# Performance work log

Measured on AMD Instinct MI355X. Metric: run time of the kernel, lower is better.

## Reference

```python
import jax, jax.numpy as jnp
import numpy as np

B, T, F, H = 256, 128, 1024, 512  # batch, input_size (time window), feature_dim, hidden_size


def setup_inputs() -> dict:
    key = jax.random.key(0)
    ks = jax.random.split(key, 7)
    in1 = T + 2 * H
    return {
        "h": jax.random.normal(ks[0], (B, H), dtype=jnp.float32),
        "s": jax.random.normal(ks[1], (B, H), dtype=jnp.float32),
        "x": jax.random.normal(ks[2], (B, T, F), dtype=jnp.float32),
        "W1": jax.random.normal(ks[3], (T, in1), dtype=jnp.float32) / np.sqrt(in1),
        "b1": jnp.zeros((T,), dtype=jnp.float32),
        "W2": jax.random.normal(ks[4], (1, T), dtype=jnp.float32) / np.sqrt(T),
        "b2": jnp.zeros((1,), dtype=jnp.float32),
    }


def reference(h, s, x, W1, b1, W2, b2):
    feature_dim = x.shape[-1]
    xp = jnp.transpose(x, (2, 0, 1))                     # [F, B, T]
    hb = jnp.broadcast_to(h[None], (feature_dim,) + h.shape)  # [F, B, H]
    sb = jnp.broadcast_to(s[None], (feature_dim,) + s.shape)  # [F, B, H]
    cat = jnp.concatenate([xp, hb, sb], axis=-1)         # [F, B, T+2H]
    u = jnp.einsum('fbk,tk->fbt', cat, W1) + b1          # [F, B, T]
    e = jnp.einsum('fbt,ot->fbo', jnp.tanh(u), W2) + b2  # [F, B, 1]
    alpha = jax.nn.softmax(e, axis=0)[..., 0]            # softmax over feature dim -> [F, B]
    return alpha.T                                       # [B, F]
```

## Files before the change

### kernel.cpp

```cpp
#include <hip/hip_runtime.h>
#include <hip/hip_bf16.h>


#define B_N 256
#define T_N 128
#define F_N 1024
#define H_N 512
#define IN1 1152

typedef __bf16 bf16x8 __attribute__((ext_vector_type(8)));
typedef float f32x16 __attribute__((ext_vector_type(16)));
typedef float f32x4_t __attribute__((ext_vector_type(4)));
typedef unsigned int u32x4 __attribute__((ext_vector_type(4)));

__device__ __forceinline__ float wave_reduce_sum(float v) {
#pragma unroll
  for (int off = 32; off >= 1; off >>= 1) v += __shfl_xor(v, off, 64);
  return v;
}
__device__ __forceinline__ float wave_reduce_max(float v) {
#pragma unroll
  for (int off = 32; off >= 1; off >>= 1) v = fmaxf(v, __shfl_xor(v, off, 64));
  return v;
}
__device__ __forceinline__ float tanh_fast(float u) {
  u = fminf(fmaxf(u, -15.f), 15.f);
  float e2 = __expf(2.f * u);
  return (e2 - 1.f) / (e2 + 1.f);
}
__device__ __forceinline__ unsigned bfbits(float f) {
  return (unsigned)__builtin_bit_cast(unsigned short, (__bf16)f);
}
__device__ __forceinline__ float dot4(float4 a, float4 b) {
  return a.x * b.x + a.y * b.y + a.z * b.z + a.w * b.w;
}

__global__ __launch_bounds__(256) void kA_c(const float* __restrict__ h,
                                            const float* __restrict__ s,
                                            const float* __restrict__ W1,
                                            const float* __restrict__ b1,
                                            float* __restrict__ c) {
  int tid = threadIdx.x, lane = tid & 63, wave = tid >> 6;
  int t = blockIdx.x >> 2, bq = blockIdx.x & 3;
  const float4* wrow = reinterpret_cast<const float4*>(W1 + (size_t)t * IN1 + T_N);
  float4 w0 = wrow[lane], w1v = wrow[64 + lane], w2v = wrow[128 + lane], w3v = wrow[192 + lane];
  float b1t = b1[t];
  int b0 = bq * 64;
#pragma unroll 2
  for (int bi = 0; bi < 16; ++bi) {
    int b = b0 + wave + bi * 4;
    const float4* hr = reinterpret_cast<const float4*>(h + (size_t)b * H_N);
    const float4* sr = reinterpret_cast<const float4*>(s + (size_t)b * H_N);
    float acc = dot4(w0, hr[lane]) + dot4(w1v, hr[64 + lane]) +
                dot4(w2v, sr[lane]) + dot4(w3v, sr[64 + lane]);
    acc = wave_reduce_sum(acc);
    if (lane == 0) c[(size_t)b * T_N + t] = acc + b1t;
  }
}

__global__ __launch_bounds__(256) void kA_frag(const float* __restrict__ W1,
                                               unsigned short* __restrict__ w1frag) {
  int i = blockIdx.x * 256 + threadIdx.x;
  int p0 = i * 2;
  int j = p0 & 7;
  int lane = (p0 >> 3) & 63;
  int kk = (p0 >> 9) & 7;
  int tt = (p0 >> 12) & 3;
  int t = tt * 32 + (lane & 31);
  int k = kk * 16 + 8 * (lane >> 5) + j;
  const float2 w = *reinterpret_cast<const float2*>(W1 + t * IN1 + k);
  *reinterpret_cast<unsigned*>(w1frag + p0) = bfbits(w.x) | (bfbits(w.y) << 16);
}

__global__ __launch_bounds__(256, 4) void kB_e(const float* __restrict__ x,
                                               const unsigned short* __restrict__ w1frag,
                                               const float* __restrict__ c,
                                               const float* __restrict__ W2,
                                               const float* __restrict__ b2,
                                               float* __restrict__ e) {
  __shared__ __align__(16) unsigned char xlds[32768];
  __shared__ __align__(16) float clds[T_N];
  __shared__ __align__(16) float w2lds[T_N];
  __shared__ __align__(16) float epart[4][T_N];
  int tid = threadIdx.x;
  int b = blockIdx.x >> 3;
  int fc = blockIdx.x & 7;
  const int fbase = fc * 128;

  if (tid < T_N) clds[tid] = c[(size_t)b * T_N + tid];
  else w2lds[tid - T_N] = W2[tid - T_N];

  {
    const float* xb = x + (size_t)b * T_N * F_N + fbase;
#pragma unroll
    for (int i = 0; i < 4; ++i) {
      int u = tid + 256 * i;
      int kq = u >> 5, fq = u & 31;
      const float* base = xb + (size_t)(kq * 4) * F_N + fq * 4;
      float4 r0 = *reinterpret_cast<const float4*>(base);
      float4 r1 = *reinterpret_cast<const float4*>(base + F_N);
      float4 r2 = *reinterpret_cast<const float4*>(base + 2 * F_N);
      float4 r3 = *reinterpret_cast<const float4*>(base + 3 * F_N);
      u32x4 pa, pb;
      pa[0] = bfbits(r0.x) | (bfbits(r1.x) << 16);
      pa[1] = bfbits(r2.x) | (bfbits(r3.x) << 16);
      pa[2] = bfbits(r0.y) | (bfbits(r1.y) << 16);
      pa[3] = bfbits(r2.y) | (bfbits(r3.y) << 16);
      pb[0] = bfbits(r0.z) | (bfbits(r1.z) << 16);
      pb[1] = bfbits(r2.z) | (bfbits(r3.z) << 16);
      pb[2] = bfbits(r0.w) | (bfbits(r1.w) << 16);
      pb[3] = bfbits(r2.w) | (bfbits(r3.w) << 16);
      unsigned char* dst = xlds + kq * 1024 + fq * 32;
      *reinterpret_cast<u32x4*>(dst) = pa;
      *reinterpret_cast<u32x4*>(dst + 16) = pb;
    }
  }
  __syncthreads();

  const int lane = tid & 63, wave = tid >> 6;
  const int g = lane >> 5, l31 = lane & 31;
  const bf16x8* af = reinterpret_cast<const bf16x8*>(w1frag);

  f32x16 acc0 = {}, acc1 = {}, acc2 = {}, acc3 = {};
#pragma unroll 4
  for (int kk = 0; kk < 8; ++kk) {
    bf16x8 afr = af[wave * 512 + kk * 64 + lane];
    const unsigned char* bbase = xlds + (kk * 4 + 2 * g) * 1024 + l31 * 8;
#define BFRAG(C)                                                                    \
  ({                                                                                \
    uint2 lo = *reinterpret_cast<const uint2*>(bbase + (C) * 256);                  \
    uint2 hi = *reinterpret_cast<const uint2*>(bbase + (C) * 256 + 1024);           \
    u32x4 q = {lo.x, lo.y, hi.x, hi.y};                                             \
    __builtin_bit_cast(bf16x8, q);                                                  \
  })
    acc0 = __builtin_amdgcn_mfma_f32_32x32x16_bf16(afr, BFRAG(0), acc0, 0, 0, 0);
    acc1 = __builtin_amdgcn_mfma_f32_32x32x16_bf16(afr, BFRAG(1), acc1, 0, 0, 0);
    acc2 = __builtin_amdgcn_mfma_f32_32x32x16_bf16(afr, BFRAG(2), acc2, 0, 0, 0);
    acc3 = __builtin_amdgcn_mfma_f32_32x32x16_bf16(afr, BFRAG(3), acc3, 0, 0, 0);
#undef BFRAG
  }

  const int tbase = wave * 32 + 4 * g;
  float es0 = 0.f, es1 = 0.f, es2 = 0.f, es3 = 0.f;
#pragma unroll
  for (int q = 0; q < 4; ++q) {
    f32x4_t cq = *reinterpret_cast<const f32x4_t*>(&clds[tbase + 8 * q]);
    f32x4_t wq = *reinterpret_cast<const f32x4_t*>(&w2lds[tbase + 8 * q]);
#pragma unroll
    for (int r = 0; r < 4; ++r) {
      int reg = q * 4 + r;
      es0 += wq[r] * tanh_fast(acc0[reg] + cq[r]);
      es1 += wq[r] * tanh_fast(acc1[reg] + cq[r]);
      es2 += wq[r] * tanh_fast(acc2[reg] + cq[r]);
      es3 += wq[r] * tanh_fast(acc3[reg] + cq[r]);
    }
  }
  es0 += __shfl_xor(es0, 32, 64);
  es1 += __shfl_xor(es1, 32, 64);
  es2 += __shfl_xor(es2, 32, 64);
  es3 += __shfl_xor(es3, 32, 64);
  if (g == 0) {
    epart[wave][l31] = es0;
    epart[wave][32 + l31] = es1;
    epart[wave][64 + l31] = es2;
    epart[wave][96 + l31] = es3;
  }
  __syncthreads();
  if (tid < T_N) {
    e[(size_t)b * F_N + fbase + tid] =
        epart[0][tid] + epart[1][tid] + epart[2][tid] + epart[3][tid] + b2[0];
  }
}

__global__ __launch_bounds__(256) void kC_softmax(float* __restrict__ out) {
  int b = blockIdx.x, tid = threadIdx.x;
  int lane = tid & 63, wid = tid >> 6;
  float* row = out + (size_t)b * F_N;
  float v[4];
#pragma unroll
  for (int q = 0; q < 4; ++q) v[q] = row[tid + 256 * q];
  float m = fmaxf(fmaxf(v[0], v[1]), fmaxf(v[2], v[3]));
  m = wave_reduce_max(m);
  __shared__ float rm[4], rs[4];
  if (lane == 0) rm[wid] = m;
  __syncthreads();
  float M = fmaxf(fmaxf(rm[0], rm[1]), fmaxf(rm[2], rm[3]));
  float ssum = 0.f;
#pragma unroll
  for (int q = 0; q < 4; ++q) {
    v[q] = __expf(v[q] - M);
    ssum += v[q];
  }
  ssum = wave_reduce_sum(ssum);
  if (lane == 0) rs[wid] = ssum;
  __syncthreads();
  float S = rs[0] + rs[1] + rs[2] + rs[3];
  float inv = 1.f / S;
#pragma unroll
  for (int q = 0; q < 4; ++q) row[tid + 256 * q] = v[q] * inv;
}

extern "C" void kernel_launch(void* const* d_in, const int* in_sizes, int n_in,
                              void* d_out, int out_size, void* d_ws, size_t ws_size,
                              hipStream_t stream) {
  const float* h = (const float*)d_in[0];
  const float* s = (const float*)d_in[1];
  const float* x = (const float*)d_in[2];
  const float* W1 = (const float*)d_in[3];
  const float* b1 = (const float*)d_in[4];
  const float* W2 = (const float*)d_in[5];
  const float* b2 = (const float*)d_in[6];
  float* out = (float*)d_out;

  float* c_ws = (float*)d_ws;
  unsigned short* w1frag = (unsigned short*)((char*)d_ws + B_N * T_N * 4);

  kA_c<<<512, 256, 0, stream>>>(h, s, W1, b1, c_ws);
  kA_frag<<<32, 256, 0, stream>>>(W1, w1frag);
  kB_e<<<2048, 256, 0, stream>>>(x, w1frag, c_ws, W2, b2, out);
  kC_softmax<<<256, 256, 0, stream>>>(out);
}
```

Measured before the change: 233.4 us.

## Halve kB_e feature tile, raise occupancy, and merge prep kernels

kB_e now gives each block 64 features instead of 128. This doubles the grid to 4096 blocks and halves the LDS tile, and the launch bound is raised to 6 blocks per CU so more waves are resident to hide x-load latency. The two preprocessing kernels (the h/s projection and the W1 fragment packing) are merged into one launch, which saves a kernel launch. In exchange, each block loads its W1 fragment again for half the useful MFMA work, and per-block setup such as the c/W2 loads is repeated twice as often.

```diff
diff --git a/kernel.cpp b/kernel.cpp
--- a/kernel.cpp
+++ b/kernel.cpp
@@ -35,57 +35,58 @@
   return a.x * b.x + a.y * b.y + a.z * b.z + a.w * b.w;
 }
 
-__global__ __launch_bounds__(256) void kA_c(const float* __restrict__ h,
-                                            const float* __restrict__ s,
-                                            const float* __restrict__ W1,
-                                            const float* __restrict__ b1,
-                                            float* __restrict__ c) {
-  int tid = threadIdx.x, lane = tid & 63, wave = tid >> 6;
-  int t = blockIdx.x >> 2, bq = blockIdx.x & 3;
-  const float4* wrow = reinterpret_cast<const float4*>(W1 + (size_t)t * IN1 + T_N);
-  float4 w0 = wrow[lane], w1v = wrow[64 + lane], w2v = wrow[128 + lane], w3v = wrow[192 + lane];
-  float b1t = b1[t];
-  int b0 = bq * 64;
+__global__ __launch_bounds__(256) void kAB(const float* __restrict__ h,
+                                           const float* __restrict__ s,
+                                           const float* __restrict__ W1,
+                                           const float* __restrict__ b1,
+                                           float* __restrict__ c,
+                                           unsigned short* __restrict__ w1frag) {
+  int tid = threadIdx.x;
+  if (blockIdx.x < 512) {
+    int lane = tid & 63, wave = tid >> 6;
+    int t = blockIdx.x >> 2, bq = blockIdx.x & 3;
+    const float4* wrow = reinterpret_cast<const float4*>(W1 + (size_t)t * IN1 + T_N);
+    float4 w0 = wrow[lane], w1v = wrow[64 + lane], w2v = wrow[128 + lane], w3v = wrow[192 + lane];
+    float b1t = b1[t];
+    int b0 = bq * 64;
 #pragma unroll 2
-  for (int bi = 0; bi < 16; ++bi) {
-    int b = b0 + wave + bi * 4;
-    const float4* hr = reinterpret_cast<const float4*>(h + (size_t)b * H_N);
-    const float4* sr = reinterpret_cast<const float4*>(s + (size_t)b * H_N);
-    float acc = dot4(w0, hr[lane]) + dot4(w1v, hr[64 + lane]) +
-                dot4(w2v, sr[lane]) + dot4(w3v, sr[64 + lane]);
-    acc = wave_reduce_sum(acc);
-    if (lane == 0) c[(size_t)b * T_N + t] = acc + b1t;
-  }
-}
-
-__global__ __launch_bounds__(256) void kA_frag(const float* __restrict__ W1,
-                                               unsigned short* __restrict__ w1frag) {
-  int i = blockIdx.x * 256 + threadIdx.x;
-  int p0 = i * 2;
-  int j = p0 & 7;
-  int lane = (p0 >> 3) & 63;
-  int kk = (p0 >> 9) & 7;
-  int tt = (p0 >> 12) & 3;
-  int t = tt * 32 + (lane & 31);
-  int k = kk * 16 + 8 * (lane >> 5) + j;
-  const float2 w = *reinterpret_cast<const float2*>(W1 + t * IN1 + k);
-  *reinterpret_cast<unsigned*>(w1frag + p0) = bfbits(w.x) | (bfbits(w.y) << 16);
-}
-
-__global__ __launch_bounds__(256, 4) void kB_e(const float* __restrict__ x,
+    for (int bi = 0; bi < 16; ++bi) {
+      int b = b0 + wave + bi * 4;
+      const float4* hr = reinterpret_cast<const float4*>(h + (size_t)b * H_N);
+      const float4* sr = reinterpret_cast<const float4*>(s + (size_t)b * H_N);
+      float acc = dot4(w0, hr[lane]) + dot4(w1v, hr[64 + lane]) +
+                  dot4(w2v, sr[lane]) + dot4(w3v, sr[64 + lane]);
+      acc = wave_reduce_sum(acc);
+      if (lane == 0) c[(size_t)b * T_N + t] = acc + b1t;
+    }
+  } else {
+    int i = (blockIdx.x - 512) * 256 + tid;
+    int p0 = i * 2;
+    int j = p0 & 7;
+    int lane = (p0 >> 3) & 63;
+    int kk = (p0 >> 9) & 7;
+    int tt = (p0 >> 12) & 3;
+    int t = tt * 32 + (lane & 31);
+    int k = kk * 16 + 8 * (lane >> 5) + j;
+    const float2 w = *reinterpret_cast<const float2*>(W1 + t * IN1 + k);
+    *reinterpret_cast<unsigned*>(w1frag + p0) = bfbits(w.x) | (bfbits(w.y) << 16);
+  }
+}
+
+__global__ __launch_bounds__(256, 6) void kB_e(const float* __restrict__ x,
                                                const unsigned short* __restrict__ w1frag,
                                                const float* __restrict__ c,
                                                const float* __restrict__ W2,
                                                const float* __restrict__ b2,
                                                float* __restrict__ e) {
-  __shared__ __align__(16) unsigned char xlds[32768];
+  __shared__ __align__(16) unsigned char xlds[16384];
   __shared__ __align__(16) float clds[T_N];
   __shared__ __align__(16) float w2lds[T_N];
-  __shared__ __align__(16) float epart[4][T_N];
+  __shared__ __align__(16) float epart[4][64];
   int tid = threadIdx.x;
-  int b = blockIdx.x >> 3;
-  int fc = blockIdx.x & 7;
-  const int fbase = fc * 128;
+  int b = blockIdx.x >> 4;
+  int fc = blockIdx.x & 15;
+  const int fbase = fc * 64;
 
   if (tid < T_N) clds[tid] = c[(size_t)b * T_N + tid];
   else w2lds[tid - T_N] = W2[tid - T_N];
@@ -93,9 +94,9 @@
   {
     const float* xb = x + (size_t)b * T_N * F_N + fbase;
 #pragma unroll
-    for (int i = 0; i < 4; ++i) {
+    for (int i = 0; i < 2; ++i) {
       int u = tid + 256 * i;
-      int kq = u >> 5, fq = u & 31;
+      int kq = u >> 4, fq = u & 15;
       const float* base = xb + (size_t)(kq * 4) * F_N + fq * 4;
       float4 r0 = *reinterpret_cast<const float4*>(base);
       float4 r1 = *reinterpret_cast<const float4*>(base + F_N);
@@ -110,7 +111,7 @@
       pb[1] = bfbits(r2.z) | (bfbits(r3.z) << 16);
       pb[2] = bfbits(r0.w) | (bfbits(r1.w) << 16);
       pb[3] = bfbits(r2.w) | (bfbits(r3.w) << 16);
-      unsigned char* dst = xlds + kq * 1024 + fq * 32;
+      unsigned char* dst = xlds + kq * 512 + fq * 32;
       *reinterpret_cast<u32x4*>(dst) = pa;
       *reinterpret_cast<u32x4*>(dst + 16) = pb;
     }
@@ -121,27 +122,25 @@
   const int g = lane >> 5, l31 = lane & 31;
   const bf16x8* af = reinterpret_cast<const bf16x8*>(w1frag);
 
-  f32x16 acc0 = {}, acc1 = {}, acc2 = {}, acc3 = {};
-#pragma unroll 4
+  f32x16 acc0 = {}, acc1 = {};
+#pragma unroll
   for (int kk = 0; kk < 8; ++kk) {
     bf16x8 afr = af[wave * 512 + kk * 64 + lane];
-    const unsigned char* bbase = xlds + (kk * 4 + 2 * g) * 1024 + l31 * 8;
+    const unsigned char* bbase = xlds + (kk * 4 + 2 * g) * 512 + l31 * 8;
 #define BFRAG(C)                                                                    \
   ({                                                                                \
     uint2 lo = *reinterpret_cast<const uint2*>(bbase + (C) * 256);                  \
-    uint2 hi = *reinterpret_cast<const uint2*>(bbase + (C) * 256 + 1024);           \
+    uint2 hi = *reinterpret_cast<const uint2*>(bbase + (C) * 256 + 512);            \
     u32x4 q = {lo.x, lo.y, hi.x, hi.y};                                             \
     __builtin_bit_cast(bf16x8, q);                                                  \
   })
     acc0 = __builtin_amdgcn_mfma_f32_32x32x16_bf16(afr, BFRAG(0), acc0, 0, 0, 0);
     acc1 = __builtin_amdgcn_mfma_f32_32x32x16_bf16(afr, BFRAG(1), acc1, 0, 0, 0);
-    acc2 = __builtin_amdgcn_mfma_f32_32x32x16_bf16(afr, BFRAG(2), acc2, 0, 0, 0);
-    acc3 = __builtin_amdgcn_mfma_f32_32x32x16_bf16(afr, BFRAG(3), acc3, 0, 0, 0);
 #undef BFRAG
   }
 
   const int tbase = wave * 32 + 4 * g;
-  float es0 = 0.f, es1 = 0.f, es2 = 0.f, es3 = 0.f;
+  float es0 = 0.f, es1 = 0.f;
 #pragma unroll
   for (int q = 0; q < 4; ++q) {
     f32x4_t cq = *reinterpret_cast<const f32x4_t*>(&clds[tbase + 8 * q]);
@@ -151,22 +150,16 @@
       int reg = q * 4 + r;
       es0 += wq[r] * tanh_fast(acc0[reg] + cq[r]);
       es1 += wq[r] * tanh_fast(acc1[reg] + cq[r]);
-      es2 += wq[r] * tanh_fast(acc2[reg] + cq[r]);
-      es3 += wq[r] * tanh_fast(acc3[reg] + cq[r]);
     }
   }
   es0 += __shfl_xor(es0, 32, 64);
   es1 += __shfl_xor(es1, 32, 64);
-  es2 += __shfl_xor(es2, 32, 64);
-  es3 += __shfl_xor(es3, 32, 64);
   if (g == 0) {
     epart[wave][l31] = es0;
     epart[wave][32 + l31] = es1;
-    epart[wave][64 + l31] = es2;
-    epart[wave][96 + l31] = es3;
-  }
-  __syncthreads();
-  if (tid < T_N) {
+  }
+  __syncthreads();
+  if (tid < 64) {
     e[(size_t)b * F_N + fbase + tid] =
         epart[0][tid] + epart[1][tid] + epart[2][tid] + epart[3][tid] + b2[0];
   }
@@ -215,8 +208,7 @@
   float* c_ws = (float*)d_ws;
   unsigned short* w1frag = (unsigned short*)((char*)d_ws + B_N * T_N * 4);
 
-  kA_c<<<512, 256, 0, stream>>>(h, s, W1, b1, c_ws);
-  kA_frag<<<32, 256, 0, stream>>>(W1, w1frag);
-  kB_e<<<2048, 256, 0, stream>>>(x, w1frag, c_ws, W2, b2, out);
+  kAB<<<544, 256, 0, stream>>>(h, s, W1, b1, c_ws, w1frag);
+  kB_e<<<4096, 256, 0, stream>>>(x, w1frag, c_ws, W2, b2, out);
   kC_softmax<<<256, 256, 0, stream>>>(out);
 }
```

Measured after the change: 225.0 us. 3.6% less time.
